# Kernel optimization log

Hardware: AMD Instinct MI355X
Metric: run time of the kernel (lower is better)

## Reference

```python
import jax, jax.numpy as jnp
import numpy as np

N_NODES = 100000
N_EDGES = 3200000
IN_FEAT = 512
HIDDEN = 16
N_CLASSES = 7


def gcn_conv(x, src, dst, dinv, W, b, n):
    # x: [N, Fin], src/dst: [E+N] (self-loops appended), dinv: [E+N already-indexed? no]
    h = x @ W  # [N, Fout]
    norm = (dinv[src] * dinv[dst])[:, None]  # [E+N, 1]
    msg = h[src] * norm
    out = jax.ops.segment_sum(msg, dst, num_segments=n)
    return out + b


def setup_inputs() -> dict:
    key = jax.random.key(0)
    k1, k2, k3, k4 = jax.random.split(key, 4)
    x = jax.random.normal(k1, (N_NODES, IN_FEAT), dtype=jnp.float32)
    edge_index = jax.random.randint(k2, (2, N_EDGES), 0, N_NODES, dtype=jnp.int64)
    # Glorot-style init for GCNConv linear layers
    W1 = jax.random.normal(k3, (IN_FEAT, HIDDEN), dtype=jnp.float32) / np.sqrt(IN_FEAT)
    b1 = jnp.zeros((HIDDEN,), dtype=jnp.float32)
    W2 = jax.random.normal(k4, (HIDDEN, N_CLASSES), dtype=jnp.float32) / np.sqrt(HIDDEN)
    b2 = jnp.zeros((N_CLASSES,), dtype=jnp.float32)
    return {"x": x, "edge_index": edge_index, "W1": W1, "b1": b1, "W2": W2, "b2": b2}


def reference(x, edge_index, W1, b1, W2, b2):
    n = x.shape[0]
    loop = jnp.arange(n, dtype=edge_index.dtype)
    src = jnp.concatenate([edge_index[0], loop])  # add self-loops (PyG default)
    dst = jnp.concatenate([edge_index[1], loop])
    # symmetric normalization: deg computed on destination with self-loops
    deg = jax.ops.segment_sum(jnp.ones_like(dst, dtype=x.dtype), dst, num_segments=n)
    dinv = jnp.where(deg > 0, jax.lax.rsqrt(deg), 0.0)
    h = gcn_conv(x, src, dst, dinv, W1, b1, n)
    h = jax.nn.relu(h)
    h = gcn_conv(h, src, dst, dinv, W2, b2, n)
    return jax.nn.log_softmax(h, axis=1)
```

## Files before the change

kernel.cpp:

```cpp
#include <hip/hip_runtime.h>

#define IN_FEAT 512
#define HID 16
#define NC 7

#define NPB    128
#define NPB_SH 7
#define NBMAX  1024
#define CAPB   5120
#define CAPS   8192
#define P1_EDGES 8192
#define P1_EPT   32

__global__ __launch_bounds__(256) void k_binmm(const int* __restrict__ src,
                                               const int* __restrict__ dst,
                                               int* __restrict__ gcur,
                                               int* __restrict__ binned,
                                               const float* __restrict__ x,
                                               const float* __restrict__ W,
                                               float* __restrict__ h1,
                                               int E, int NB, int nchunk, int n, int gN) {
    int tid = threadIdx.x;
    int idx = blockIdx.x;
    int twice = 2 * (nchunk < gN ? nchunk : gN);
    bool isBin;
    int ridx;
    if (idx < twice) { isBin = !(idx & 1); ridx = idx >> 1; }
    else {
        int r = idx - twice;
        if (nchunk > gN) { isBin = true;  ridx = gN + r; }
        else             { isBin = false; ridx = nchunk + r; }
    }

    if (isBin) {
        __shared__ int lcur[NBMAX];
        __shared__ int sbase[NBMAX];
        for (int b = tid; b < NB; b += 256) lcur[b] = 0;
        __syncthreads();

        int base = ridx * P1_EDGES + tid;
        int d[P1_EPT];
        int lp[P1_EPT];
#pragma unroll
        for (int i = 0; i < P1_EPT; ++i) {
            int e = base + i * 256;
            d[i] = (e < E) ? __builtin_nontemporal_load(dst + e) : -1;
        }
#pragma unroll
        for (int i = 0; i < P1_EPT; ++i) {
            if (d[i] >= 0) lp[i] = atomicAdd(&lcur[d[i] >> NPB_SH], 1);
        }
        __syncthreads();
        for (int b = tid; b < NB; b += 256) {
            int c = lcur[b];
            sbase[b] = c ? atomicAdd(&gcur[b], c) : 0;
        }
        __syncthreads();
#pragma unroll
        for (int i = 0; i < P1_EPT; ++i) {
            if (d[i] < 0) continue;
            int e = base + i * 256;
            int s = __builtin_nontemporal_load(src + e);
            int b = d[i] >> NPB_SH;
            int pos = sbase[b] + lp[i];
            if (pos < CAPB)
                binned[(size_t)b * CAPB + pos] = s | ((d[i] & (NPB - 1)) << 20);
        }
    } else {
        int row = ridx * 256 + tid;
        if (row >= n) return;
        const float4* xr = reinterpret_cast<const float4*>(x + (size_t)row * IN_FEAT);
        float acc[HID];
#pragma unroll
        for (int c = 0; c < HID; ++c) acc[c] = 0.0f;
        for (int kt0 = 0; kt0 < IN_FEAT / 4; kt0 += 8) {
            float4 xv[8];
#pragma unroll
            for (int j = 0; j < 8; ++j) xv[j] = xr[kt0 + j];
#pragma unroll
            for (int j = 0; j < 8; ++j) {
                const float* wk = W + (size_t)(kt0 + j) * 4 * HID;
#pragma unroll
                for (int c = 0; c < HID; ++c) acc[c] = fmaf(xv[j].x, wk[c], acc[c]);
#pragma unroll
                for (int c = 0; c < HID; ++c) acc[c] = fmaf(xv[j].y, wk[HID + c], acc[c]);
#pragma unroll
                for (int c = 0; c < HID; ++c) acc[c] = fmaf(xv[j].z, wk[2 * HID + c], acc[c]);
#pragma unroll
                for (int c = 0; c < HID; ++c) acc[c] = fmaf(xv[j].w, wk[3 * HID + c], acc[c]);
            }
        }
        float4* hp = reinterpret_cast<float4*>(h1 + (size_t)row * HID);
#pragma unroll
        for (int j = 0; j < 4; ++j)
            hp[j] = make_float4(acc[4 * j], acc[4 * j + 1], acc[4 * j + 2], acc[4 * j + 3]);
    }
}

__global__ __launch_bounds__(256) void k_sort2(const int* __restrict__ binned,
                                               const int* __restrict__ gcur,
                                               int* __restrict__ off,
                                               float* __restrict__ dinv,
                                               int* __restrict__ csr,
                                               const int* __restrict__ src,
                                               const int* __restrict__ dst,
                                               int n, int E, int NB) {
    __shared__ int hist[NPB];
    __shared__ int hoff[NPB];
    __shared__ int cur[NPB];
    __shared__ int wtot[4];
    __shared__ int s_base;
    __shared__ int stage[CAPS];
    int b = blockIdx.x;
    int lo = b << NPB_SH;
    int nn = min(NPB, n - lo);
    int tid = threadIdx.x;
    int lane = tid & 63, wid = tid >> 6;
    int tot = gcur[b];

    int pre = 0;
    for (int k = tid; k < b; k += 256) pre += gcur[k];
#pragma unroll
    for (int o = 32; o >= 1; o >>= 1) pre += __shfl_xor(pre, o, 64);
    if (lane == 0) wtot[wid] = pre;
    if (tid < NPB) { hist[tid] = 0; cur[tid] = 0; }
    __syncthreads();
    if (tid == 0) s_base = wtot[0] + wtot[1] + wtot[2] + wtot[3];
    __syncthreads();
    int base = s_base;
    bool fits = (tot <= CAPB) && (tot <= CAPS);

    const int* bb = binned + (size_t)b * CAPB;
    if (fits) {
        for (int k = tid; k < tot; k += 256)
            atomicAdd(&hist[(bb[k] >> 20) & (NPB - 1)], 1);
    } else {
        for (int e = tid; e < E; e += 256) {
            int dd = dst[e];
            if ((dd >> NPB_SH) == b) atomicAdd(&hist[dd & (NPB - 1)], 1);
        }
    }
    __syncthreads();

    int v = 0, incl = 0;
    if (tid < NPB) {
        v = hist[tid];
        incl = v;
#pragma unroll
        for (int o = 1; o < 64; o <<= 1) {
            int t = __shfl_up(incl, o, 64);
            if ((tid & 63) >= o) incl += t;
        }
        if ((tid & 63) == 63) wtot[tid >> 6] = incl;
    }
    __syncthreads();
    if (tid < NPB) {
        int ex = incl - v + ((tid >= 64) ? wtot[0] : 0);
        hoff[tid] = ex;
        if (tid < nn) {
            off[lo + tid] = base + ex;
            dinv[lo + tid] = rsqrtf((float)v + 1.0f);
        }
    }
    if (b == NB - 1 && tid == 0) off[n] = base + tot;
    __syncthreads();

    if (fits) {
        for (int k = tid; k < tot; k += 256) {
            int e = bb[k];
            int dl = (e >> 20) & (NPB - 1);
            int p = hoff[dl] + atomicAdd(&cur[dl], 1);
            stage[p] = e & 0xFFFFF;
        }
        __syncthreads();
        for (int k = tid; k < tot; k += 256) csr[base + k] = stage[k];
    } else {
        for (int e = tid; e < E; e += 256) {
            int dd = dst[e];
            if ((dd >> NPB_SH) == b) {
                int dl = dd & (NPB - 1);
                int p = base + hoff[dl] + atomicAdd(&cur[dl], 1);
                csr[p] = src[e];
            }
        }
    }
}

__global__ void k_gather1(const float* __restrict__ h1, const int* __restrict__ csr_src,
                          const int* __restrict__ off, const float* __restrict__ dinv,
                          const float* __restrict__ b1, const float* __restrict__ W2,
                          float* __restrict__ h2, int n) {
    int t = blockIdx.x * blockDim.x + threadIdx.x;
    int v = t >> 2, part = t & 3;
    if (v >= n) return;
    float di = dinv[v];
    float4 hv = reinterpret_cast<const float4*>(h1 + (size_t)v * HID)[part];
    float dw = di * di;
    float4 acc = make_float4(hv.x * dw, hv.y * dw, hv.z * dw, hv.w * dw);
    int beg = off[v], end = off[v + 1];
    for (int i = beg; i < end; ++i) {
        int s = csr_src[i];
        float w = dinv[s] * di;
        float4 hs = reinterpret_cast<const float4*>(h1 + (size_t)s * HID)[part];
        acc.x = fmaf(hs.x, w, acc.x);
        acc.y = fmaf(hs.y, w, acc.y);
        acc.z = fmaf(hs.z, w, acc.z);
        acc.w = fmaf(hs.w, w, acc.w);
    }
    float tt[4];
    tt[0] = fmaxf(acc.x + b1[part * 4 + 0], 0.0f);
    tt[1] = fmaxf(acc.y + b1[part * 4 + 1], 0.0f);
    tt[2] = fmaxf(acc.z + b1[part * 4 + 2], 0.0f);
    tt[3] = fmaxf(acc.w + b1[part * 4 + 3], 0.0f);
    float o[NC];
#pragma unroll
    for (int c = 0; c < NC; ++c) o[c] = 0.0f;
#pragma unroll
    for (int j = 0; j < 4; ++j) {
        int k = part * 4 + j;
#pragma unroll
        for (int c = 0; c < NC; ++c) o[c] = fmaf(tt[j], W2[k * NC + c], o[c]);
    }
#pragma unroll
    for (int c = 0; c < NC; ++c) {
        o[c] += __shfl_xor(o[c], 1);
        o[c] += __shfl_xor(o[c], 2);
    }
    float4* hp = reinterpret_cast<float4*>(h2 + (size_t)v * 8);
    if (part == 0) hp[0] = make_float4(o[0], o[1], o[2], o[3]);
    if (part == 1) hp[1] = make_float4(o[4], o[5], o[6], 0.0f);
}

__global__ void k_gather2(const float* __restrict__ h2, const int* __restrict__ csr_src,
                          const int* __restrict__ off, const float* __restrict__ dinv,
                          const float* __restrict__ b2, float* __restrict__ out, int n) {
    int v = blockIdx.x * blockDim.x + threadIdx.x;
    if (v >= n) return;
    float di = dinv[v];
    float dw = di * di;
    const float4* hr = reinterpret_cast<const float4*>(h2 + (size_t)v * 8);
    float4 s0 = hr[0], s1 = hr[1];
    float4 a0 = make_float4(s0.x * dw, s0.y * dw, s0.z * dw, s0.w * dw);
    float4 a1 = make_float4(s1.x * dw, s1.y * dw, s1.z * dw, 0.0f);
    int beg = off[v], end = off[v + 1];
    for (int i = beg; i < end; ++i) {
        int s = csr_src[i];
        float w = dinv[s] * di;
        const float4* hs = reinterpret_cast<const float4*>(h2 + (size_t)s * 8);
        float4 v0 = hs[0], v1 = hs[1];
        a0.x = fmaf(v0.x, w, a0.x);
        a0.y = fmaf(v0.y, w, a0.y);
        a0.z = fmaf(v0.z, w, a0.z);
        a0.w = fmaf(v0.w, w, a0.w);
        a1.x = fmaf(v1.x, w, a1.x);
        a1.y = fmaf(v1.y, w, a1.y);
        a1.z = fmaf(v1.z, w, a1.z);
    }
    float z[NC];
    z[0] = a0.x + b2[0]; z[1] = a0.y + b2[1]; z[2] = a0.z + b2[2]; z[3] = a0.w + b2[3];
    z[4] = a1.x + b2[4]; z[5] = a1.y + b2[5]; z[6] = a1.z + b2[6];
    float m = z[0];
#pragma unroll
    for (int c = 1; c < NC; ++c) m = fmaxf(m, z[c]);
    float sum = 0.0f;
#pragma unroll
    for (int c = 0; c < NC; ++c) sum += expf(z[c] - m);
    float lse = logf(sum) + m;
#pragma unroll
    for (int c = 0; c < NC; ++c) out[(size_t)v * NC + c] = z[c] - lse;
}

extern "C" void kernel_launch(void* const* d_in, const int* in_sizes, int n_in,
                              void* d_out, int out_size, void* d_ws, size_t ws_size,
                              hipStream_t stream) {
    const float* x  = (const float*)d_in[0];
    const int*   ei = (const int*)d_in[1];
    const float* W1 = (const float*)d_in[2];
    const float* b1 = (const float*)d_in[3];
    const float* W2 = (const float*)d_in[4];
    const float* b2 = (const float*)d_in[5];

    int n = in_sizes[0] / IN_FEAT;
    int E = in_sizes[1] / 2;
    const int* src = ei;
    const int* dst = ei + E;
    int NB = (n + NPB - 1) >> NPB_SH;

    char* p = (char*)d_ws;
    int*   binned  = (int*)p;     p += (size_t)NB * CAPB * sizeof(int);
    float* h1      = (float*)p;   p += (size_t)HID * n * sizeof(float);
    float* h2      = (float*)p;   p += (size_t)8 * n * sizeof(float);
    int*   csr_src = (int*)p;     p += (size_t)E * sizeof(int);
    int*   gcur    = (int*)p;     p += (size_t)NBMAX * sizeof(int);
    int*   off     = (int*)p;     p += (size_t)(n + 1) * sizeof(int);
    float* dinv    = (float*)p;   p += (size_t)n * sizeof(float);

    const int tb = 256;
    int gN = (n + tb - 1) / tb;
    int gN4 = (4 * n + tb - 1) / tb;
    int nchunk = (E + P1_EDGES - 1) / P1_EDGES;

    hipMemsetAsync(gcur, 0, (size_t)NBMAX * sizeof(int), stream);
    k_binmm  <<<nchunk + gN, tb, 0, stream>>>(src, dst, gcur, binned, x, W1, h1,
                                              E, NB, nchunk, n, gN);
    k_sort2  <<<NB, tb, 0, stream>>>(binned, gcur, off, dinv, csr_src,
                                     src, dst, n, E, NB);
    k_gather1<<<gN4, tb, 0, stream>>>(h1, csr_src, off, dinv, b1, W2, h2, n);
    k_gather2<<<gN,  tb, 0, stream>>>(h2, csr_src, off, dinv, b2, (float*)d_out, n);
}
```

Before: 261.6 us.

## Split GEMM K across waves and store h1 in fp16 for gather

```diff
diff --git a/kernel.cpp b/kernel.cpp
--- a/kernel.cpp
+++ b/kernel.cpp
@@ -1,4 +1,5 @@
 #include <hip/hip_runtime.h>
+#include <hip/hip_fp16.h>
 
 #define IN_FEAT 512
 #define HID 16
@@ -18,18 +19,19 @@
                                                int* __restrict__ binned,
                                                const float* __restrict__ x,
                                                const float* __restrict__ W,
-                                               float* __restrict__ h1,
-                                               int E, int NB, int nchunk, int n, int gN) {
+                                               __half* __restrict__ h1,
+                                               int E, int NB, int nchunk, int n, int gGem) {
     int tid = threadIdx.x;
     int idx = blockIdx.x;
-    int twice = 2 * (nchunk < gN ? nchunk : gN);
+    int mn = (nchunk < gGem ? nchunk : gGem);
+    int twice = 2 * mn;
     bool isBin;
     int ridx;
     if (idx < twice) { isBin = !(idx & 1); ridx = idx >> 1; }
     else {
         int r = idx - twice;
-        if (nchunk > gN) { isBin = true;  ridx = gN + r; }
-        else             { isBin = false; ridx = nchunk + r; }
+        if (nchunk > gGem) { isBin = true;  ridx = mn + r; }
+        else               { isBin = false; ridx = mn + r; }
     }
 
     if (isBin) {
@@ -67,33 +69,57 @@
                 binned[(size_t)b * CAPB + pos] = s | ((d[i] & (NPB - 1)) << 20);
         }
     } else {
-        int row = ridx * 256 + tid;
-        if (row >= n) return;
-        const float4* xr = reinterpret_cast<const float4*>(x + (size_t)row * IN_FEAT);
-        float acc[HID];
-#pragma unroll
-        for (int c = 0; c < HID; ++c) acc[c] = 0.0f;
-        for (int kt0 = 0; kt0 < IN_FEAT / 4; kt0 += 8) {
-            float4 xv[8];
-#pragma unroll
-            for (int j = 0; j < 8; ++j) xv[j] = xr[kt0 + j];
-#pragma unroll
-            for (int j = 0; j < 8; ++j) {
-                const float* wk = W + (size_t)(kt0 + j) * 4 * HID;
-#pragma unroll
-                for (int c = 0; c < HID; ++c) acc[c] = fmaf(xv[j].x, wk[c], acc[c]);
-#pragma unroll
-                for (int c = 0; c < HID; ++c) acc[c] = fmaf(xv[j].y, wk[HID + c], acc[c]);
-#pragma unroll
-                for (int c = 0; c < HID; ++c) acc[c] = fmaf(xv[j].z, wk[2 * HID + c], acc[c]);
-#pragma unroll
-                for (int c = 0; c < HID; ++c) acc[c] = fmaf(xv[j].w, wk[3 * HID + c], acc[c]);
+        __shared__ float lacc[128][HID + 1];
+        for (int q = tid; q < 128 * (HID + 1); q += 256)
+            (&lacc[0][0])[q] = 0.0f;
+        __syncthreads();
+
+        int w = tid >> 6, lane = tid & 63;
+        int lo = ridx * 128;
+        int lr = (w & 1) * 64 + lane;
+        int row = lo + lr;
+        int khalf = w >> 1;
+        if (row < n) {
+            const float4* xr = reinterpret_cast<const float4*>(x + (size_t)row * IN_FEAT)
+                             + khalf * 64;
+            float acc[HID];
+#pragma unroll
+            for (int c = 0; c < HID; ++c) acc[c] = 0.0f;
+            for (int kt0 = 0; kt0 < 64; kt0 += 8) {
+                float4 xv[8];
+#pragma unroll
+                for (int j = 0; j < 8; ++j) xv[j] = xr[kt0 + j];
+#pragma unroll
+                for (int j = 0; j < 8; ++j) {
+                    const float* wk = W + (size_t)(khalf * 64 + kt0 + j) * 4 * HID;
+#pragma unroll
+                    for (int c = 0; c < HID; ++c) acc[c] = fmaf(xv[j].x, wk[c], acc[c]);
+#pragma unroll
+                    for (int c = 0; c < HID; ++c) acc[c] = fmaf(xv[j].y, wk[HID + c], acc[c]);
+#pragma unroll
+                    for (int c = 0; c < HID; ++c) acc[c] = fmaf(xv[j].z, wk[2 * HID + c], acc[c]);
+#pragma unroll
+                    for (int c = 0; c < HID; ++c) acc[c] = fmaf(xv[j].w, wk[3 * HID + c], acc[c]);
+                }
             }
-        }
-        float4* hp = reinterpret_cast<float4*>(h1 + (size_t)row * HID);
-#pragma unroll
-        for (int j = 0; j < 4; ++j)
-            hp[j] = make_float4(acc[4 * j], acc[4 * j + 1], acc[4 * j + 2], acc[4 * j + 3]);
+#pragma unroll
+            for (int c = 0; c < HID; ++c) atomicAdd(&lacc[lr][c], acc[c]);
+        }
+        __syncthreads();
+        if (tid < 128) {
+            int r2 = lo + tid;
+            if (r2 < n) {
+                unsigned u[8];
+#pragma unroll
+                for (int j = 0; j < 8; ++j) {
+                    __half2 hh = __floats2half2_rn(lacc[tid][2 * j], lacc[tid][2 * j + 1]);
+                    u[j] = *reinterpret_cast<unsigned*>(&hh);
+                }
+                uint4* hp = reinterpret_cast<uint4*>(h1 + (size_t)r2 * HID);
+                hp[0] = make_uint4(u[0], u[1], u[2], u[3]);
+                hp[1] = make_uint4(u[4], u[5], u[6], u[7]);
+            }
+        }
     }
 }
 
@@ -186,7 +212,7 @@
     }
 }
 
-__global__ void k_gather1(const float* __restrict__ h1, const int* __restrict__ csr_src,
+__global__ void k_gather1(const __half* __restrict__ h1, const int* __restrict__ csr_src,
                           const int* __restrict__ off, const float* __restrict__ dinv,
                           const float* __restrict__ b1, const float* __restrict__ W2,
                           float* __restrict__ h2, int n) {
@@ -194,18 +220,24 @@
     int v = t >> 2, part = t & 3;
     if (v >= n) return;
     float di = dinv[v];
-    float4 hv = reinterpret_cast<const float4*>(h1 + (size_t)v * HID)[part];
     float dw = di * di;
-    float4 acc = make_float4(hv.x * dw, hv.y * dw, hv.z * dw, hv.w * dw);
+    uint2 raw = *reinterpret_cast<const uint2*>(h1 + (size_t)v * HID + part * 4);
+    __half2 q0 = *reinterpret_cast<__half2*>(&raw.x);
+    __half2 q1 = *reinterpret_cast<__half2*>(&raw.y);
+    float2 f0 = __half22float2(q0), f1 = __half22float2(q1);
+    float4 acc = make_float4(f0.x * dw, f0.y * dw, f1.x * dw, f1.y * dw);
     int beg = off[v], end = off[v + 1];
     for (int i = beg; i < end; ++i) {
         int s = csr_src[i];
         float w = dinv[s] * di;
-        float4 hs = reinterpret_cast<const float4*>(h1 + (size_t)s * HID)[part];
-        acc.x = fmaf(hs.x, w, acc.x);
-        acc.y = fmaf(hs.y, w, acc.y);
-        acc.z = fmaf(hs.z, w, acc.z);
-        acc.w = fmaf(hs.w, w, acc.w);
+        uint2 r2 = *reinterpret_cast<const uint2*>(h1 + (size_t)s * HID + part * 4);
+        __half2 a0 = *reinterpret_cast<__half2*>(&r2.x);
+        __half2 a1 = *reinterpret_cast<__half2*>(&r2.y);
+        float2 g0 = __half22float2(a0), g1 = __half22float2(a1);
+        acc.x = fmaf(g0.x, w, acc.x);
+        acc.y = fmaf(g0.y, w, acc.y);
+        acc.z = fmaf(g1.x, w, acc.z);
+        acc.w = fmaf(g1.y, w, acc.w);
     }
     float tt[4];
     tt[0] = fmaxf(acc.x + b1[part * 4 + 0], 0.0f);
@@ -287,22 +319,23 @@
     int NB = (n + NPB - 1) >> NPB_SH;
 
     char* p = (char*)d_ws;
-    int*   binned  = (int*)p;     p += (size_t)NB * CAPB * sizeof(int);
-    float* h1      = (float*)p;   p += (size_t)HID * n * sizeof(float);
-    float* h2      = (float*)p;   p += (size_t)8 * n * sizeof(float);
-    int*   csr_src = (int*)p;     p += (size_t)E * sizeof(int);
-    int*   gcur    = (int*)p;     p += (size_t)NBMAX * sizeof(int);
-    int*   off     = (int*)p;     p += (size_t)(n + 1) * sizeof(int);
-    float* dinv    = (float*)p;   p += (size_t)n * sizeof(float);
+    int*    binned  = (int*)p;    p += (size_t)NB * CAPB * sizeof(int);
+    __half* h1      = (__half*)p; p += (size_t)HID * n * sizeof(__half);
+    float*  h2      = (float*)p;  p += (size_t)8 * n * sizeof(float);
+    int*    csr_src = (int*)p;    p += (size_t)E * sizeof(int);
+    int*    gcur    = (int*)p;    p += (size_t)NBMAX * sizeof(int);
+    int*    off     = (int*)p;    p += (size_t)(n + 1) * sizeof(int);
+    float*  dinv    = (float*)p;  p += (size_t)n * sizeof(float);
 
     const int tb = 256;
     int gN = (n + tb - 1) / tb;
     int gN4 = (4 * n + tb - 1) / tb;
+    int gGem = (n + 127) / 128;
     int nchunk = (E + P1_EDGES - 1) / P1_EDGES;
 
     hipMemsetAsync(gcur, 0, (size_t)NBMAX * sizeof(int), stream);
-    k_binmm  <<<nchunk + gN, tb, 0, stream>>>(src, dst, gcur, binned, x, W1, h1,
-                                              E, NB, nchunk, n, gN);
+    k_binmm  <<<nchunk + gGem, tb, 0, stream>>>(src, dst, gcur, binned, x, W1, h1,
+                                                E, NB, nchunk, n, gGem);
     k_sort2  <<<NB, tb, 0, stream>>>(binned, gcur, off, dinv, csr_src,
                                      src, dst, n, E, NB);
     k_gather1<<<gN4, tb, 0, stream>>>(h1, csr_src, off, dinv, b1, W2, h2, n);
```

Result: slower. 342.8 us (+31.0%).
